# Kernel tuning notes

Measured on AMD Instinct MI355X. Metric: run time of the kernel, lower is better.

Reference implementation:

```python
import jax, jax.numpy as jnp
import numpy as np

N_NODES = 100000
N_EDGES = 3200000
F_IN, F_HID, F_OUT = 61, 16, 2  # num_features, hidden, num_classes
K = 2  # kernel_size (dim=1, degree=1 linear open B-spline)


def spline_conv(x, src, dst, u, W, root, bias, n_nodes):
    """SplineConv, dim=1, kernel_size=2, degree=1, open spline, aggr='mean'.
    Linear B-spline basis on u in [0,1]: B0 = 1-u, B1 = u.
    Since the basis depends only on the edge and the transform is linear,
    precompute both node-level transforms then gather+blend per edge.
    W: [K, f_in, f_out], root: [f_in, f_out], bias: [f_out].
    """
    h = jnp.einsum('nf,kfc->knc', x, W)  # [K, N, f_out] (tiny matmuls)
    w1 = u[:, 0]            # [E]
    w0 = 1.0 - w1
    msg = w0[:, None] * h[0][src] + w1[:, None] * h[1][src]  # [E, f_out]
    summed = jax.ops.segment_sum(msg, dst, num_segments=n_nodes)
    cnt = jax.ops.segment_sum(jnp.ones((msg.shape[0],), msg.dtype), dst,
                              num_segments=n_nodes)
    out = summed / jnp.maximum(cnt, 1.0)[:, None]            # mean aggregation
    return out + x @ root + bias


def setup_inputs() -> dict:
    key = jax.random.key(0)
    ks = jax.random.split(key, 9)
    x = jax.random.normal(ks[0], (N_NODES, F_IN), dtype=jnp.float32)
    edge_index = jax.random.randint(ks[1], (2, N_EDGES), 0, N_NODES, dtype=jnp.int64)
    edge_attr = jax.random.uniform(ks[2], (N_EDGES, 1), dtype=jnp.float32)
    s1 = 1.0 / np.sqrt(F_IN)
    s2 = 1.0 / np.sqrt(F_HID)
    W1 = jax.random.normal(ks[3], (K, F_IN, F_HID), dtype=jnp.float32) * s1
    root1 = jax.random.normal(ks[4], (F_IN, F_HID), dtype=jnp.float32) * s1
    b1 = jnp.zeros((F_HID,), jnp.float32)
    W2 = jax.random.normal(ks[5], (K, F_HID, F_OUT), dtype=jnp.float32) * s2
    root2 = jax.random.normal(ks[6], (F_HID, F_OUT), dtype=jnp.float32) * s2
    b2 = jnp.zeros((F_OUT,), jnp.float32)
    return {"x": x, "edge_index": edge_index, "edge_attr": edge_attr,
            "dropout": 0, "W1": W1, "root1": root1, "b1": b1,
            "W2": W2, "root2": root2, "b2": b2}


def reference(x, edge_index, edge_attr, dropout, W1, root1, b1, W2, root2, b2):
    # Eval mode: F.dropout(training=False) is identity; `dropout` arg is unused
    # in the original forward body.
    src, dst = edge_index[0], edge_index[1]
    n = x.shape[0]
    h = spline_conv(x, src, dst, edge_attr, W1, root1, b1, n)
    h = jax.nn.elu(h)
    h = spline_conv(h, src, dst, edge_attr, W2, root2, b2, n)
    return jax.nn.log_softmax(h, axis=1)
```

## Files before the change

kernel.cpp:

```cpp
#include <hip/hip_runtime.h>
#include <hip/hip_fp16.h>
#include <hip/hip_fp8.h>

#define N_NODES 100000
#define N_EDGES 3200000
#define F_IN    61
#define F_HID   16
#define F_OUT   2
#define HB      256
#define CHUNK   (N_EDGES / HB)
#define BSIZE   512
#define NBUCK   196
#define RPT     17
#define FCAP    (1024 * RPT)

typedef unsigned int uint;


__global__ __launch_bounds__(256) void k_transform1(
    const float* __restrict__ x, const float* __restrict__ W1,
    const float* __restrict__ root1, const float* __restrict__ b1,
    uint2* __restrict__ hp8, float* __restrict__ r1)
{
    __shared__ float w0s[F_IN * F_HID];
    __shared__ float w1s[F_IN * F_HID];
    __shared__ float rs [F_IN * F_HID];
    __shared__ float bs [F_HID];

    const int tid = threadIdx.x;
    for (int i = tid; i < F_IN * F_HID; i += 256) {
        w0s[i] = W1[i];
        w1s[i] = W1[F_IN * F_HID + i];
        rs[i]  = root1[i];
    }
    if (tid < F_HID) bs[tid] = b1[tid];
    __syncthreads();

    const int j = tid & 3;
    const int n = (blockIdx.x * 256 + tid) >> 2;
    if (n >= N_NODES) return;

    float a0[F_HID], a1[F_HID], ar[F_HID];
    #pragma unroll
    for (int c = 0; c < F_HID; ++c) { a0[c] = 0.f; a1[c] = 0.f; ar[c] = 0.f; }

    const float* xr = x + (size_t)n * F_IN;
    for (int f = j; f < F_IN; f += 4) {
        const float xv = xr[f];
        #pragma unroll
        for (int c = 0; c < F_HID; ++c) {
            a0[c] = fmaf(xv, w0s[f * F_HID + c], a0[c]);
            a1[c] = fmaf(xv, w1s[f * F_HID + c], a1[c]);
            ar[c] = fmaf(xv, rs [f * F_HID + c], ar[c]);
        }
    }

    #pragma unroll
    for (int c = 0; c < F_HID; ++c) {
        a0[c] += __shfl_xor(a0[c], 1); a0[c] += __shfl_xor(a0[c], 2);
        a1[c] += __shfl_xor(a1[c], 1); a1[c] += __shfl_xor(a1[c], 2);
        ar[c] += __shfl_xor(ar[c], 1); ar[c] += __shfl_xor(ar[c], 2);
    }

    const int c0 = 4 * j;
    __hip_fp8x4_e4m3 p0(make_float4(a0[c0 + 0], a1[c0 + 0], a0[c0 + 1], a1[c0 + 1]));
    __hip_fp8x4_e4m3 p1(make_float4(a0[c0 + 2], a1[c0 + 2], a0[c0 + 3], a1[c0 + 3]));
    uint2 w;
    w.x = (uint)p0.__x;
    w.y = (uint)p1.__x;
    hp8[(size_t)n * 4 + j] = w;

    float4 rv = make_float4(ar[c0 + 0] + bs[c0 + 0], ar[c0 + 1] + bs[c0 + 1],
                            ar[c0 + 2] + bs[c0 + 2], ar[c0 + 3] + bs[c0 + 3]);
    ((float4*)r1)[(size_t)n * 4 + j] = rv;
}

__global__ __launch_bounds__(1024) void k_bhist(
    const int* __restrict__ edst, uint* __restrict__ cnt)
{
    __shared__ uint bins[2][NBUCK];
    uint* fb = &bins[0][0];
    const int bx = blockIdx.x, tid = threadIdx.x;
    for (int i = tid; i < 2 * NBUCK; i += 1024) fb[i] = 0;
    __syncthreads();
    const int e0 = bx * CHUNK, e1 = e0 + CHUNK;
    const int sb = tid & 1;
    for (int e = e0 + tid; e < e1; e += 1024)
        atomicAdd(&bins[sb][((uint)edst[e]) >> 9], 1u);
    __syncthreads();
    for (int i = tid; i < NBUCK; i += 1024)
        cnt[(size_t)i * HB + bx] = bins[0][i] + bins[1][i];
}

__global__ __launch_bounds__(256) void k_brow1(
    uint* __restrict__ cnt, uint* __restrict__ tot)
{
    __shared__ uint s[256];
    const int b = blockIdx.x, tid = threadIdx.x;
    const uint v = cnt[(size_t)b * HB + tid];
    s[tid] = v; __syncthreads();
    for (int off = 1; off < 256; off <<= 1) {
        const uint t = (tid >= off) ? s[tid - off] : 0u;
        __syncthreads();
        s[tid] += t;
        __syncthreads();
    }
    cnt[(size_t)b * HB + tid] = s[tid] - v;
    if (tid == 255) tot[b] = s[255];
}

__global__ __launch_bounds__(256) void k_bexc(
    const uint* __restrict__ tot, uint* __restrict__ bstart)
{
    __shared__ uint s[256];
    const int tid = threadIdx.x;
    const uint v = (tid < NBUCK) ? tot[tid] : 0u;
    s[tid] = v; __syncthreads();
    for (int off = 1; off < 256; off <<= 1) {
        const uint t = (tid >= off) ? s[tid - off] : 0u;
        __syncthreads();
        s[tid] += t;
        __syncthreads();
    }
    if (tid < NBUCK) bstart[tid] = s[tid] - v;
    if (tid == 0) bstart[NBUCK] = N_EDGES;
}

__global__ __launch_bounds__(1024) void k_bscatter(
    const int* __restrict__ esrc, const int* __restrict__ edst,
    const float* __restrict__ attr, const uint* __restrict__ cnt,
    const uint* __restrict__ bstart, uint* __restrict__ buck)
{
    __shared__ uint pos[NBUCK];
    const int bx = blockIdx.x, tid = threadIdx.x;
    for (int i = tid; i < NBUCK; i += 1024)
        pos[i] = cnt[(size_t)i * HB + bx] + bstart[i];
    __syncthreads();
    const int e0 = bx * CHUNK, e1 = e0 + CHUNK;
    for (int e = e0 + tid; e < e1; e += 1024) {
        const uint d = (uint)edst[e];
        const uint uq = (uint)(attr[e] * 63.0f + 0.5f);
        const uint p = atomicAdd(&pos[d >> 9], 1u);
        buck[p] = ((uint)esrc[e] << 15) | ((d & 511u) << 6) | uq;
    }
}

__global__ __launch_bounds__(1024) void k_fscatter(
    const uint* __restrict__ buck, const uint* __restrict__ bstart,
    uint* __restrict__ rowptr, uint* __restrict__ vals)
{
    __shared__ uint deg[BSIZE];
    __shared__ uint excl[BSIZE];
    const int b = blockIdx.x, tid = threadIdx.x;
    const uint e0 = bstart[b], e1 = bstart[b + 1];
    const bool fits = (e1 - e0) <= (uint)FCAP;

    for (int i = tid; i < BSIZE; i += 1024) deg[i] = 0;
    __syncthreads();

    uint r[RPT];
    if (fits) {
        #pragma unroll
        for (int k = 0; k < RPT; ++k) {
            const uint e = e0 + (uint)tid + (uint)k * 1024u;
            if (e < e1) r[k] = buck[e];
        }
        #pragma unroll
        for (int k = 0; k < RPT; ++k) {
            const uint e = e0 + (uint)tid + (uint)k * 1024u;
            if (e < e1) atomicAdd(&deg[(r[k] >> 6) & 511u], 1u);
        }
    } else {
        for (uint e = e0 + tid; e < e1; e += 1024)
            atomicAdd(&deg[(buck[e] >> 6) & 511u], 1u);
    }
    __syncthreads();

    if (tid < BSIZE) excl[tid] = deg[tid];
    __syncthreads();
    for (int off = 1; off < BSIZE; off <<= 1) {
        uint t = 0;
        if (tid < BSIZE && tid >= off) t = excl[tid - off];
        __syncthreads();
        if (tid < BSIZE) excl[tid] += t;
        __syncthreads();
    }
    if (tid < BSIZE) {
        const uint ex = excl[tid] - deg[tid];
        const int n = b * BSIZE + tid;
        if (n < N_NODES) rowptr[n] = e0 + ex;
        deg[tid] = ex;
    }
    if (b == 0 && tid == 0) rowptr[N_NODES] = N_EDGES;
    __syncthreads();

    if (fits) {
        #pragma unroll
        for (int k = 0; k < RPT; ++k) {
            const uint e = e0 + (uint)tid + (uint)k * 1024u;
            if (e < e1) {
                const uint p = atomicAdd(&deg[(r[k] >> 6) & 511u], 1u);
                vals[e0 + p] = r[k];
            }
        }
    } else {
        for (uint e = e0 + tid; e < e1; e += 1024) {
            const uint w = buck[e];
            const uint p = atomicAdd(&deg[(w >> 6) & 511u], 1u);
            vals[e0 + p] = w;
        }
    }
}

__global__ __launch_bounds__(256) void k_agg1(
    const uint* __restrict__ rowptr, const uint* __restrict__ vals,
    const uint* __restrict__ hp8, float2* __restrict__ sum1)
{
    __shared__ uint2 ent[4][64];
    const int tid = threadIdx.x;
    const int lane = tid & 63;
    const int wave = tid >> 6;
    const int n = blockIdx.x * 4 + wave;
    const int ep = lane >> 3;
    const int q  = lane & 7;

    const uint r0 = rowptr[n];
    const uint deg = rowptr[n + 1] - r0;
    const uint dcap = min(deg, 64u);

    if ((uint)lane < dcap) {
        const uint v = __builtin_nontemporal_load(&vals[r0 + lane]);
        const float uu = (float)(v & 63u) * (1.0f / 63.0f);
        ent[wave][lane] = make_uint2(v >> 15, __float_as_uint(uu));
    }
    __syncthreads();

    float acc_a = 0.f, acc_b = 0.f;
    #pragma unroll 4
    for (uint i = ep; i < dcap; i += 8) {
        const uint2 e = ent[wave][i];
        const float u = __uint_as_float(e.y);
        const float w0 = 1.0f - u;
        __hip_fp8x4_e4m3 p;
        p.__x = (__hip_fp8x4_storage_t)hp8[(size_t)e.x * 8 + q];
        const float4 h = (float4)p;
        acc_a += w0 * h.x + u * h.y;
        acc_b += w0 * h.z + u * h.w;
    }
    for (uint i = 64 + ep; i < deg; i += 8) {
        const uint v = __builtin_nontemporal_load(&vals[r0 + i]);
        const float u = (float)(v & 63u) * (1.0f / 63.0f);
        const float w0 = 1.0f - u;
        __hip_fp8x4_e4m3 p;
        p.__x = (__hip_fp8x4_storage_t)hp8[(size_t)(v >> 15) * 8 + q];
        const float4 h = (float4)p;
        acc_a += w0 * h.x + u * h.y;
        acc_b += w0 * h.z + u * h.w;
    }
    acc_a += __shfl_xor(acc_a, 8); acc_a += __shfl_xor(acc_a, 16); acc_a += __shfl_xor(acc_a, 32);
    acc_b += __shfl_xor(acc_b, 8); acc_b += __shfl_xor(acc_b, 16); acc_b += __shfl_xor(acc_b, 32);

    if (lane < 8)
        sum1[(size_t)n * 8 + lane] = make_float2(acc_a, acc_b);
}

__global__ __launch_bounds__(256) void k_mid2(
    const float2* __restrict__ sum1, const uint* __restrict__ rowptr,
    const float* __restrict__ r1,
    const float* __restrict__ W2, const float* __restrict__ root2,
    const float* __restrict__ b2,
    float4* __restrict__ h2, float2* __restrict__ r2)
{
    __shared__ float w2s[2 * F_HID * F_OUT];
    __shared__ float rts[F_HID * F_OUT];
    __shared__ float b2s[F_OUT];
    const int tid = threadIdx.x;
    if (tid < 2 * F_HID * F_OUT) w2s[tid] = W2[tid];
    if (tid < F_HID * F_OUT)     rts[tid] = root2[tid];
    if (tid < F_OUT)             b2s[tid] = b2[tid];
    __syncthreads();

    const int n = blockIdx.x * 256 + tid;
    if (n >= N_NODES) return;

    const uint deg = rowptr[n + 1] - rowptr[n];
    const float inv = 1.0f / (float)max(deg, 1u);

    float h[F_HID];
    #pragma unroll
    for (int k = 0; k < 8; ++k) {
        const float2 s = sum1[(size_t)n * 8 + k];
        const float v0 = s.x * inv + r1[(size_t)n * F_HID + 2 * k];
        const float v1 = s.y * inv + r1[(size_t)n * F_HID + 2 * k + 1];
        h[2 * k]     = (v0 > 0.0f) ? v0 : expm1f(v0);
        h[2 * k + 1] = (v1 > 0.0f) ? v1 : expm1f(v1);
    }
    float o00 = 0.f, o01 = 0.f, o10 = 0.f, o11 = 0.f;
    float rr0 = b2s[0], rr1 = b2s[1];
    #pragma unroll
    for (int f = 0; f < F_HID; ++f) {
        o00 = fmaf(h[f], w2s[f * 2 + 0], o00);
        o01 = fmaf(h[f], w2s[f * 2 + 1], o01);
        o10 = fmaf(h[f], w2s[2 * F_HID + f * 2 + 0], o10);
        o11 = fmaf(h[f], w2s[2 * F_HID + f * 2 + 1], o11);
        rr0 = fmaf(h[f], rts[f * 2 + 0], rr0);
        rr1 = fmaf(h[f], rts[f * 2 + 1], rr1);
    }
    h2[n] = make_float4(o00, o10, o01, o11);
    r2[n] = make_float2(rr0, rr1);
}

__global__ __launch_bounds__(256) void k_agg2(
    const uint* __restrict__ rowptr, const uint* __restrict__ vals,
    const float4* __restrict__ h2, const float2* __restrict__ r2,
    float2* __restrict__ out)
{
    const int tid  = threadIdx.x;
    const int lane = tid & 63;
    const int wave = tid >> 6;
    const int half = lane & 31;
    const int n = blockIdx.x * 8 + wave * 2 + (lane >> 5);

    const uint r0 = rowptr[n];
    const uint deg = rowptr[n + 1] - r0;

    float acc0 = 0.f, acc1 = 0.f;
    for (uint i = half; i < deg; i += 32) {
        const uint v = __builtin_nontemporal_load(&vals[r0 + i]);
        const float uu = (float)(v & 63u) * (1.0f / 63.0f);
        const float4 h = h2[v >> 15];
        acc0 += (1.0f - uu) * h.x + uu * h.y;
        acc1 += (1.0f - uu) * h.z + uu * h.w;
    }
    #pragma unroll
    for (int off = 1; off <= 16; off <<= 1) {
        acc0 += __shfl_xor(acc0, off);
        acc1 += __shfl_xor(acc1, off);
    }

    if (half == 0) {
        const float inv = 1.0f / (float)max(deg, 1u);
        const float2 rr = r2[n];
        const float o0 = acc0 * inv + rr.x;
        const float o1 = acc1 * inv + rr.y;
        const float m  = fmaxf(o0, o1);
        const float l  = m + logf(expf(o0 - m) + expf(o1 - m));
        out[n] = make_float2(o0 - l, o1 - l);
    }
}

extern "C" void kernel_launch(void* const* d_in, const int* in_sizes, int n_in,
                              void* d_out, int out_size, void* d_ws, size_t ws_size,
                              hipStream_t stream) {
    const float* x     = (const float*)d_in[0];
    const int*   ei    = (const int*)  d_in[1];
    const float* attr  = (const float*)d_in[2];
    const float* W1    = (const float*)d_in[4];
    const float* root1 = (const float*)d_in[5];
    const float* b1    = (const float*)d_in[6];
    const float* W2    = (const float*)d_in[7];
    const float* root2 = (const float*)d_in[8];
    const float* b2    = (const float*)d_in[9];
    float2* out = (float2*)d_out;

    char* ws = (char*)d_ws;
    size_t off = 0;
    uint*  vals   = (uint*) (ws + off); off += (size_t)N_EDGES * sizeof(uint);
    uint*  rowptr = (uint*) (ws + off); off += (size_t)(N_NODES + 1) * sizeof(uint);
    uint*  cnt    = (uint*) (ws + off); off += (size_t)NBUCK * HB * sizeof(uint);
    uint*  bstart = (uint*) (ws + off); off += (size_t)(NBUCK + 1) * sizeof(uint);
    uint*  tot    = (uint*) (ws + off); off += (size_t)NBUCK * sizeof(uint);
    off = (off + 255) & ~(size_t)255;
    uint*  buck   = (uint*) (ws + off); off += (size_t)N_EDGES * sizeof(uint);

    char* alias = (char*)buck;
    size_t aoff = 0;
    uint2*  hp8 = (uint2*) (alias + aoff); aoff += (size_t)N_NODES * 4 * sizeof(uint2);
    float*   r1 = (float*) (alias + aoff); aoff += (size_t)N_NODES * F_HID * sizeof(float);
    float4*  h2 = (float4*)(alias + aoff); aoff += (size_t)N_NODES * sizeof(float4);
    float2*  r2 = (float2*)(alias + aoff); aoff += (size_t)N_NODES * sizeof(float2);
    float2* sum1= (float2*)(alias + aoff); aoff += (size_t)N_NODES * 8 * sizeof(float2);
    (void)ws_size;

    const int* esrc = ei;
    const int* edst = ei + N_EDGES;

    k_bhist    <<<HB, 1024, 0, stream>>>(edst, cnt);
    k_brow1    <<<NBUCK, 256, 0, stream>>>(cnt, tot);
    k_bexc     <<<1, 256, 0, stream>>>(tot, bstart);
    k_bscatter <<<HB, 1024, 0, stream>>>(esrc, edst, attr, cnt, bstart, buck);
    k_fscatter <<<NBUCK, 1024, 0, stream>>>(buck, bstart, rowptr, vals);
    k_transform1<<<(N_NODES * 4 + 255) / 256, 256, 0, stream>>>(x, W1, root1, b1, hp8, r1);
    k_agg1     <<<N_NODES / 4, 256, 0, stream>>>(rowptr, vals, (const uint*)hp8, sum1);
    k_mid2     <<<(N_NODES + 255) / 256, 256, 0, stream>>>(sum1, rowptr, r1, W2, root2, b2, h2, r2);
    k_agg2     <<<N_NODES / 8, 256, 0, stream>>>(rowptr, vals, h2, r2, out);
}
```

Measured before the change: 164.0 us.

## Fuse layer-1 aggregation with ELU and layer-2 node transform

The k_mid2 node-transform kernel is merged into k_agg1, so each wave finishes the mean, ELU and the small 16x2 projections right after its edge reduction. This drops the sum1 round trip through global memory and one kernel launch. The lane mapping also changes: each edge is now handled by 4 lanes loading uint2 (8 fp8 values) instead of 8 lanes loading uint, with 16 edges in flight per wave. This costs extra shuffle reductions and some idle lanes in the epilogue.

```diff
diff --git a/kernel.cpp b/kernel.cpp
--- a/kernel.cpp
+++ b/kernel.cpp
@@ -214,63 +214,12 @@
 
 __global__ __launch_bounds__(256) void k_agg1(
     const uint* __restrict__ rowptr, const uint* __restrict__ vals,
-    const uint* __restrict__ hp8, float2* __restrict__ sum1)
-{
-    __shared__ uint2 ent[4][64];
-    const int tid = threadIdx.x;
-    const int lane = tid & 63;
-    const int wave = tid >> 6;
-    const int n = blockIdx.x * 4 + wave;
-    const int ep = lane >> 3;
-    const int q  = lane & 7;
-
-    const uint r0 = rowptr[n];
-    const uint deg = rowptr[n + 1] - r0;
-    const uint dcap = min(deg, 64u);
-
-    if ((uint)lane < dcap) {
-        const uint v = __builtin_nontemporal_load(&vals[r0 + lane]);
-        const float uu = (float)(v & 63u) * (1.0f / 63.0f);
-        ent[wave][lane] = make_uint2(v >> 15, __float_as_uint(uu));
-    }
-    __syncthreads();
-
-    float acc_a = 0.f, acc_b = 0.f;
-    #pragma unroll 4
-    for (uint i = ep; i < dcap; i += 8) {
-        const uint2 e = ent[wave][i];
-        const float u = __uint_as_float(e.y);
-        const float w0 = 1.0f - u;
-        __hip_fp8x4_e4m3 p;
-        p.__x = (__hip_fp8x4_storage_t)hp8[(size_t)e.x * 8 + q];
-        const float4 h = (float4)p;
-        acc_a += w0 * h.x + u * h.y;
-        acc_b += w0 * h.z + u * h.w;
-    }
-    for (uint i = 64 + ep; i < deg; i += 8) {
-        const uint v = __builtin_nontemporal_load(&vals[r0 + i]);
-        const float u = (float)(v & 63u) * (1.0f / 63.0f);
-        const float w0 = 1.0f - u;
-        __hip_fp8x4_e4m3 p;
-        p.__x = (__hip_fp8x4_storage_t)hp8[(size_t)(v >> 15) * 8 + q];
-        const float4 h = (float4)p;
-        acc_a += w0 * h.x + u * h.y;
-        acc_b += w0 * h.z + u * h.w;
-    }
-    acc_a += __shfl_xor(acc_a, 8); acc_a += __shfl_xor(acc_a, 16); acc_a += __shfl_xor(acc_a, 32);
-    acc_b += __shfl_xor(acc_b, 8); acc_b += __shfl_xor(acc_b, 16); acc_b += __shfl_xor(acc_b, 32);
-
-    if (lane < 8)
-        sum1[(size_t)n * 8 + lane] = make_float2(acc_a, acc_b);
-}
-
-__global__ __launch_bounds__(256) void k_mid2(
-    const float2* __restrict__ sum1, const uint* __restrict__ rowptr,
-    const float* __restrict__ r1,
+    const uint2* __restrict__ hp8, const float4* __restrict__ r1v4,
     const float* __restrict__ W2, const float* __restrict__ root2,
     const float* __restrict__ b2,
     float4* __restrict__ h2, float2* __restrict__ r2)
 {
+    __shared__ uint2 ent[4][64];
     __shared__ float w2s[2 * F_HID * F_OUT];
     __shared__ float rts[F_HID * F_OUT];
     __shared__ float b2s[F_OUT];
@@ -278,36 +227,95 @@
     if (tid < 2 * F_HID * F_OUT) w2s[tid] = W2[tid];
     if (tid < F_HID * F_OUT)     rts[tid] = root2[tid];
     if (tid < F_OUT)             b2s[tid] = b2[tid];
-    __syncthreads();
-
-    const int n = blockIdx.x * 256 + tid;
-    if (n >= N_NODES) return;
-
-    const uint deg = rowptr[n + 1] - rowptr[n];
+
+    const int lane = tid & 63;
+    const int wave = tid >> 6;
+    const int n = blockIdx.x * 4 + wave;
+    const int ep = lane >> 2;
+    const int q  = lane & 3;
+
+    const uint r0 = rowptr[n];
+    const uint deg = rowptr[n + 1] - r0;
+    const uint dcap = min(deg, 64u);
+
+    if ((uint)lane < dcap) {
+        const uint v = __builtin_nontemporal_load(&vals[r0 + lane]);
+        const float uu = (float)(v & 63u) * (1.0f / 63.0f);
+        ent[wave][lane] = make_uint2(v >> 15, __float_as_uint(uu));
+    }
+    __syncthreads();
+
+    float4 acc = make_float4(0.f, 0.f, 0.f, 0.f);
+    #pragma unroll 2
+    for (uint i = ep; i < dcap; i += 16) {
+        const uint2 e = ent[wave][i];
+        const float u = __uint_as_float(e.y);
+        const float w0 = 1.0f - u;
+        const uint2 hw = hp8[(size_t)e.x * 4 + q];
+        __hip_fp8x4_e4m3 p0, p1;
+        p0.__x = (__hip_fp8x4_storage_t)hw.x;
+        p1.__x = (__hip_fp8x4_storage_t)hw.y;
+        const float4 f0 = (float4)p0;
+        const float4 f1 = (float4)p1;
+        acc.x += w0 * f0.x + u * f0.y;
+        acc.y += w0 * f0.z + u * f0.w;
+        acc.z += w0 * f1.x + u * f1.y;
+        acc.w += w0 * f1.z + u * f1.w;
+    }
+    for (uint i = 64 + ep; i < deg; i += 16) {
+        const uint v = __builtin_nontemporal_load(&vals[r0 + i]);
+        const float u = (float)(v & 63u) * (1.0f / 63.0f);
+        const float w0 = 1.0f - u;
+        const uint2 hw = hp8[(size_t)(v >> 15) * 4 + q];
+        __hip_fp8x4_e4m3 p0, p1;
+        p0.__x = (__hip_fp8x4_storage_t)hw.x;
+        p1.__x = (__hip_fp8x4_storage_t)hw.y;
+        const float4 f0 = (float4)p0;
+        const float4 f1 = (float4)p1;
+        acc.x += w0 * f0.x + u * f0.y;
+        acc.y += w0 * f0.z + u * f0.w;
+        acc.z += w0 * f1.x + u * f1.y;
+        acc.w += w0 * f1.z + u * f1.w;
+    }
+
+    #pragma unroll
+    for (int off = 4; off <= 32; off <<= 1) {
+        acc.x += __shfl_xor(acc.x, off);
+        acc.y += __shfl_xor(acc.y, off);
+        acc.z += __shfl_xor(acc.z, off);
+        acc.w += __shfl_xor(acc.w, off);
+    }
+
     const float inv = 1.0f / (float)max(deg, 1u);
-
-    float h[F_HID];
-    #pragma unroll
-    for (int k = 0; k < 8; ++k) {
-        const float2 s = sum1[(size_t)n * 8 + k];
-        const float v0 = s.x * inv + r1[(size_t)n * F_HID + 2 * k];
-        const float v1 = s.y * inv + r1[(size_t)n * F_HID + 2 * k + 1];
-        h[2 * k]     = (v0 > 0.0f) ? v0 : expm1f(v0);
-        h[2 * k + 1] = (v1 > 0.0f) ? v1 : expm1f(v1);
-    }
-    float o00 = 0.f, o01 = 0.f, o10 = 0.f, o11 = 0.f;
-    float rr0 = b2s[0], rr1 = b2s[1];
-    #pragma unroll
-    for (int f = 0; f < F_HID; ++f) {
-        o00 = fmaf(h[f], w2s[f * 2 + 0], o00);
-        o01 = fmaf(h[f], w2s[f * 2 + 1], o01);
-        o10 = fmaf(h[f], w2s[2 * F_HID + f * 2 + 0], o10);
-        o11 = fmaf(h[f], w2s[2 * F_HID + f * 2 + 1], o11);
-        rr0 = fmaf(h[f], rts[f * 2 + 0], rr0);
-        rr1 = fmaf(h[f], rts[f * 2 + 1], rr1);
-    }
-    h2[n] = make_float4(o00, o10, o01, o11);
-    r2[n] = make_float2(rr0, rr1);
+    const float4 rv = r1v4[(size_t)n * 4 + q];
+    float h0 = acc.x * inv + rv.x; h0 = (h0 > 0.f) ? h0 : expm1f(h0);
+    float h1 = acc.y * inv + rv.y; h1 = (h1 > 0.f) ? h1 : expm1f(h1);
+    float hc2 = acc.z * inv + rv.z; hc2 = (hc2 > 0.f) ? hc2 : expm1f(hc2);
+    float h3 = acc.w * inv + rv.w; h3 = (h3 > 0.f) ? h3 : expm1f(h3);
+
+    const int c0 = 4 * q;
+    float o00 = 0.f, o01 = 0.f, o10 = 0.f, o11 = 0.f, rr0 = 0.f, rr1 = 0.f;
+    const float hh[4] = {h0, h1, hc2, h3};
+    #pragma unroll
+    for (int k = 0; k < 4; ++k) {
+        const int c = c0 + k;
+        o00 = fmaf(hh[k], w2s[c * 2 + 0], o00);
+        o01 = fmaf(hh[k], w2s[c * 2 + 1], o01);
+        o10 = fmaf(hh[k], w2s[2 * F_HID + c * 2 + 0], o10);
+        o11 = fmaf(hh[k], w2s[2 * F_HID + c * 2 + 1], o11);
+        rr0 = fmaf(hh[k], rts[c * 2 + 0], rr0);
+        rr1 = fmaf(hh[k], rts[c * 2 + 1], rr1);
+    }
+    #pragma unroll
+    for (int off = 1; off <= 2; off <<= 1) {
+        o00 += __shfl_xor(o00, off); o01 += __shfl_xor(o01, off);
+        o10 += __shfl_xor(o10, off); o11 += __shfl_xor(o11, off);
+        rr0 += __shfl_xor(rr0, off); rr1 += __shfl_xor(rr1, off);
+    }
+    if (lane == 0) {
+        h2[n] = make_float4(o00, o10, o01, o11);
+        r2[n] = make_float2(rr0 + b2s[0], rr1 + b2s[1]);
+    }
 }
 
 __global__ __launch_bounds__(256) void k_agg2(
@@ -379,7 +387,6 @@
     float*   r1 = (float*) (alias + aoff); aoff += (size_t)N_NODES * F_HID * sizeof(float);
     float4*  h2 = (float4*)(alias + aoff); aoff += (size_t)N_NODES * sizeof(float4);
     float2*  r2 = (float2*)(alias + aoff); aoff += (size_t)N_NODES * sizeof(float2);
-    float2* sum1= (float2*)(alias + aoff); aoff += (size_t)N_NODES * 8 * sizeof(float2);
     (void)ws_size;
 
     const int* esrc = ei;
@@ -391,7 +398,7 @@
     k_bscatter <<<HB, 1024, 0, stream>>>(esrc, edst, attr, cnt, bstart, buck);
     k_fscatter <<<NBUCK, 1024, 0, stream>>>(buck, bstart, rowptr, vals);
     k_transform1<<<(N_NODES * 4 + 255) / 256, 256, 0, stream>>>(x, W1, root1, b1, hp8, r1);
-    k_agg1     <<<N_NODES / 4, 256, 0, stream>>>(rowptr, vals, (const uint*)hp8, sum1);
-    k_mid2     <<<(N_NODES + 255) / 256, 256, 0, stream>>>(sum1, rowptr, r1, W2, root2, b2, h2, r2);
+    k_agg1     <<<N_NODES / 4, 256, 0, stream>>>(rowptr, vals, hp8, (const float4*)r1,
+                                                 W2, root2, b2, h2, r2);
     k_agg2     <<<N_NODES / 8, 256, 0, stream>>>(rowptr, vals, h2, r2, out);
 }
```

New measurement: 172.7 us. +5.3%, slower.
